# Kernel optimization log

Measured on AMD Instinct MI355X. Metric: run time of the kernel, lower is better.

## Reference

```python
import jax, jax.numpy as jnp
import numpy as np

FC = 8  # heads_count
EPS = 1e-12  # torch F.normalize eps


def setup_inputs() -> dict:
    key = jax.random.key(0)
    ks = jax.random.split(key, 8)
    n, l, s, C, H = 4, 4096, 256, 256, 256
    return {
        "x0": jax.random.normal(ks[0], (n, l, C), jnp.float32),
        "center1": jax.random.normal(ks[1], (n, s, C), jnp.float32),
        "W0": jax.random.normal(ks[2], (H, C), jnp.float32) * 0.05,
        "b0": jax.random.normal(ks[3], (H,), jnp.float32) * 0.05,
        "W1": jax.random.normal(ks[4], (2 * H, C), jnp.float32) * 0.05,
        "b1": jax.random.normal(ks[5], (2 * H,), jnp.float32) * 0.05,
        "Wm": jax.random.normal(ks[6], (C, H), jnp.float32) * 0.05,
        "bm": jax.random.normal(ks[7], (C,), jnp.float32) * 0.05,
        "alpha": jnp.ones((1,), jnp.float32),
        "beta": jnp.zeros((1,), jnp.float32),
    }


def _l2norm(x):
    # matches torch F.normalize(dim=-1): x / max(||x||, eps)
    nrm = jnp.sqrt(jnp.sum(x * x, axis=-1, keepdims=True))
    return x / jnp.maximum(nrm, EPS)


def reference(x0, center1, W0, b0, W1, b1, Wm, bm, alpha, beta):
    n, l, c = x0.shape
    s = center1.shape[1]
    H = W0.shape[0]
    sc = H // FC
    m = n * FC
    # projections
    x0p = x0 @ W0.T + b0                        # [n, l, H]
    c1 = center1 @ W1.T + b1                    # [n, s, 2H]
    # split heads: 'n l (fc sc) -> (n fc) l sc'
    x0p = x0p.reshape(n, l, FC, sc).transpose(0, 2, 1, 3).reshape(m, l, sc)
    c1 = c1.reshape(n, s, FC, 2 * sc).transpose(0, 2, 1, 3).reshape(m, s, 2 * sc)
    c_point, c_value = c1[..., :sc], c1[..., sc:]
    # cosine similarity + affine + sigmoid
    sim = jnp.einsum('mlc,msc->mls', _l2norm(x0p), _l2norm(c_point))
    sim = jax.nn.sigmoid(alpha[0] * sim + beta[0])
    # top-1 hard routing
    max_vals = jnp.max(sim, axis=2)             # [m, l]
    max_idx = jnp.argmax(sim, axis=2)           # [m, l]
    gathered = jnp.take_along_axis(c_value, max_idx[:, :, None], axis=1)  # [m, l, sc]
    dispatched = max_vals[:, :, None] * gathered
    # '(n fc) l sc -> n l (fc sc)'
    dispatched = dispatched.reshape(n, FC, l, sc).transpose(0, 2, 1, 3).reshape(n, l, H)
    return dispatched @ Wm.T + bm               # [n, l, c]
```

## Files before the change

### kernel.cpp

```cpp
#include <hip/hip_runtime.h>
#include <math.h>

#define Nn 4
#define Ll 4096
#define Ss 256
#define Cc 256
#define FC 8
#define SC 32

typedef __attribute__((ext_vector_type(8))) short short8;
typedef __attribute__((ext_vector_type(8))) _Float16 half8;
typedef __attribute__((ext_vector_type(4))) float f32x4;

__device__ __forceinline__ unsigned short f2bf(float x) {
  unsigned int u = __float_as_uint(x);
  return (unsigned short)((u + 0x7FFFu + ((u >> 16) & 1u)) >> 16);
}

__device__ __forceinline__ void split8v(float4 a, float4 b,
                                        half8& hi, half8& lo) {
  float v[8] = {a.x, a.y, a.z, a.w, b.x, b.y, b.z, b.w};
#pragma unroll
  for (int i = 0; i < 8; i++) {
    float x = v[i];
    _Float16 h = (_Float16)x;
    float r = (x - (float)h) * 2048.f;
    hi[i] = h;
    lo[i] = (_Float16)r;
  }
}

#define PROJ_LOAD(Abuf, Bbuf, KOFF)                                     \
  {                                                                     \
    _Pragma("unroll")                                                   \
    for (int mi = 0; mi < 4; mi++) {                                    \
      const float* p = Ab + (size_t)mi * 16 * Cc + (KOFF);              \
      Abuf[mi][0] = *(const float4*)p;                                  \
      Abuf[mi][1] = *(const float4*)(p + 4);                            \
    }                                                                   \
    _Pragma("unroll")                                                   \
    for (int ni = 0; ni < 2; ni++) {                                    \
      const float* p = Bb + (size_t)ni * 16 * Cc + (KOFF);              \
      Bbuf[ni][0] = *(const float4*)p;                                  \
      Bbuf[ni][1] = *(const float4*)(p + 4);                            \
    }                                                                   \
  }

#define PROJ_COMPUTE(Abuf, Bbuf)                                        \
  {                                                                     \
    half8 Bh[2], Bl[2];                                                 \
    _Pragma("unroll")                                                   \
    for (int ni = 0; ni < 2; ni++)                                      \
      split8v(Bbuf[ni][0], Bbuf[ni][1], Bh[ni], Bl[ni]);                \
    _Pragma("unroll")                                                   \
    for (int mi = 0; mi < 4; mi++) {                                    \
      half8 Ah, Al;                                                     \
      split8v(Abuf[mi][0], Abuf[mi][1], Ah, Al);                        \
      _Pragma("unroll")                                                 \
      for (int ni = 0; ni < 2; ni++) {                                  \
        acc1[mi][ni] = __builtin_amdgcn_mfma_f32_16x16x32_f16(          \
            Ah, Bh[ni], acc1[mi][ni], 0, 0, 0);                         \
        acc2[mi][ni] = __builtin_amdgcn_mfma_f32_16x16x32_f16(          \
            Ah, Bl[ni], acc2[mi][ni], 0, 0, 0);                         \
        acc2[mi][ni] = __builtin_amdgcn_mfma_f32_16x16x32_f16(          \
            Al, Bh[ni], acc2[mi][ni], 0, 0, 0);                         \
      }                                                                 \
    }                                                                   \
  }

__device__ __forceinline__ void mfma_core_f32(
    const float* __restrict__ A, const float* __restrict__ B,
    const float* __restrict__ bias, size_t m0w, int n0w, int lane,
    f32x4 acc1[4][2], f32x4 acc2[4][2]) {
  int quad = lane >> 4, l15 = lane & 15;
#pragma unroll
  for (int ni = 0; ni < 2; ni++) {
    float bv = bias[n0w + ni * 16 + l15];
    f32x4 ci = {bv, bv, bv, bv};
    f32x4 zz = {0.f, 0.f, 0.f, 0.f};
#pragma unroll
    for (int mi = 0; mi < 4; mi++) { acc1[mi][ni] = ci; acc2[mi][ni] = zz; }
  }
  const float* Ab = A + (m0w + l15) * Cc + quad * 8;
  const float* Bb = B + (size_t)(n0w + l15) * Cc + quad * 8;

  float4 cA[4][2], cB[2][2], nA[4][2], nB[2][2];
  PROJ_LOAD(cA, cB, 0);
#pragma unroll 1
  for (int kt = 0; kt < 8; kt += 2) {
    PROJ_LOAD(nA, nB, (kt + 1) * 32);
    PROJ_COMPUTE(cA, cB);
    if (kt < 6) PROJ_LOAD(cA, cB, (kt + 2) * 32);
    PROJ_COMPUTE(nA, nB);
  }
}

__global__ __launch_bounds__(256, 2) void proj_mfma_k(
    const float* __restrict__ x0, const float* __restrict__ W0,
    const float* __restrict__ b0, const float* __restrict__ center1,
    const float* __restrict__ W1, const float* __restrict__ b1,
    float* __restrict__ xn, float* __restrict__ cpn, float* __restrict__ cval) {
  int t = threadIdx.x;
  int wave = t >> 6, lane = t & 63;
  int quad = lane >> 4, l15 = lane & 15;
  int b = blockIdx.x;
  f32x4 acc1[4][2], acc2[4][2];

  if (b < 512) {
    int r = (b & 7) + 8 * ((b >> 3) & 15);
    int cb = b >> 7;
    size_t m0 = (size_t)r * 128 + (size_t)(wave & 1) * 64;
    int n0 = cb * 64 + (wave >> 1) * 32;
    mfma_core_f32(x0, W0, b0, m0, n0, lane, acc1, acc2);
#pragma unroll
    for (int mi = 0; mi < 4; mi++) {
#pragma unroll
      for (int reg = 0; reg < 4; reg++) {
        size_t row = m0 + mi * 16 + quad * 4 + reg;
        float* orow = xn + row * Cc + n0;
#pragma unroll
        for (int ni = 0; ni < 2; ni++)
          orow[ni * 16 + l15] =
              acc1[mi][ni][reg] + acc2[mi][ni][reg] * (1.f / 2048.f);
      }
    }
  } else {
    int b2 = b - 512;
    size_t m0 = (size_t)(b2 >> 3) * 128 + (size_t)(wave & 1) * 64;
    int n0 = (b2 & 7) * 64 + (wave >> 1) * 32;
    mfma_core_f32(center1, W1, b1, m0, n0, lane, acc1, acc2);
    int f = n0 >> 6;
    bool point = (n0 & 32) == 0;
#pragma unroll
    for (int mi = 0; mi < 4; mi++) {
#pragma unroll
      for (int reg = 0; reg < 4; reg++) {
        int row = (int)m0 + mi * 16 + quad * 4 + reg;
        int nI = row >> 8, s = row & 255;
        float v0 = acc1[mi][0][reg] + acc2[mi][0][reg] * (1.f / 2048.f);
        float v1 = acc1[mi][1][reg] + acc2[mi][1][reg] * (1.f / 2048.f);
        size_t base = (((size_t)nI * FC + f) * Ss + s) * SC;
        if (point) {
          float ss = v0 * v0 + v1 * v1;
          ss += __shfl_xor(ss, 1, 64);
          ss += __shfl_xor(ss, 2, 64);
          ss += __shfl_xor(ss, 4, 64);
          ss += __shfl_xor(ss, 8, 64);
          float rin = 1.f / fmaxf(sqrtf(ss), 1e-12f);
          cpn[base + l15] = v0 * rin;
          cpn[base + 16 + l15] = v1 * rin;
        } else {
          cval[base + l15] = v0;
          cval[base + 16 + l15] = v1;
        }
      }
    }
  }
}

__global__ __launch_bounds__(256) void sim_k(
    float* __restrict__ xn, const float* __restrict__ cpn,
    const float* __restrict__ cval, const float* __restrict__ alphap,
    const float* __restrict__ betap) {
  __shared__ half8 BhS[4][256];
  __shared__ half8 BlS[4][256];
  int t = threadIdx.x;
  int wave = t >> 6, lane = t & 63;
  int quad = lane >> 4, l15 = lane & 15;
  int lt = blockIdx.x & 63;
  int nf = blockIdx.x >> 6;
  int f = nf & 7, nI = nf >> 3;
  int l0 = lt * 64;
  const float* cp = cpn + (size_t)nf * Ss * SC;

  {
    int s = t;
    float4 va[8];
#pragma unroll
    for (int q8 = 0; q8 < 8; q8++)
      va[q8] = *(const float4*)(cp + (size_t)s * SC + q8 * 4);
#pragma unroll
    for (int q = 0; q < 4; q++) {
      half8 h, l;
      split8v(va[2 * q], va[2 * q + 1], h, l);
      BhS[q][s] = h;
      BlS[q][s] = l;
    }
  }

  half8 Ah, Al;
  {
    const float* xrow =
        xn + ((size_t)nI * Ll + l0 + wave * 16 + l15) * Cc + f * SC + quad * 8;
    float4 a0 = *(const float4*)xrow;
    float4 a1 = *(const float4*)(xrow + 4);
    float ssq = a0.x * a0.x + a0.y * a0.y + a0.z * a0.z + a0.w * a0.w +
                a1.x * a1.x + a1.y * a1.y + a1.z * a1.z + a1.w * a1.w;
    ssq += __shfl_xor(ssq, 16, 64);
    ssq += __shfl_xor(ssq, 32, 64);
    float rin = 1.f / fmaxf(sqrtf(ssq), 1e-12f);
    a0.x *= rin; a0.y *= rin; a0.z *= rin; a0.w *= rin;
    a1.x *= rin; a1.y *= rin; a1.z *= rin; a1.w *= rin;
    split8v(a0, a1, Ah, Al);
  }

  __syncthreads();

  float a = alphap[0], bt = betap[0];
  float best[4];
  int bi[4];
#pragma unroll
  for (int r = 0; r < 4; r++) { best[r] = -3.0e38f; bi[r] = 0; }

#pragma unroll
  for (int j = 0; j < 16; j++) {
    half8 bh = BhS[quad][j * 16 + l15];
    half8 bl = BlS[quad][j * 16 + l15];
    f32x4 z = {0.f, 0.f, 0.f, 0.f};
    f32x4 c1 = __builtin_amdgcn_mfma_f32_16x16x32_f16(Ah, bh, z, 0, 0, 0);
    f32x4 c2 = __builtin_amdgcn_mfma_f32_16x16x32_f16(Ah, bl, z, 0, 0, 0);
    c2 = __builtin_amdgcn_mfma_f32_16x16x32_f16(Al, bh, c2, 0, 0, 0);
    int s = j * 16 + l15;
#pragma unroll
    for (int r = 0; r < 4; r++) {
      float v = c1[r] + c2[r] * (1.f / 2048.f);
      float tv = fmaf(a, v, bt);
      if (tv > best[r]) { best[r] = tv; bi[r] = s; }
    }
  }

#pragma unroll
  for (int r = 0; r < 4; r++) {
    float bv = best[r];
    int ix = bi[r];
#pragma unroll
    for (int m = 1; m <= 8; m <<= 1) {
      float ov = __shfl_xor(bv, m, 64);
      int oi = __shfl_xor(ix, m, 64);
      if (ov > bv || (ov == bv && oi < ix)) { bv = ov; ix = oi; }
    }
    float mv = 1.f / (1.f + expf(-bv));
    const float* cvp = cval + ((size_t)nf * Ss + ix) * SC;
    float* orow =
        xn + ((size_t)nI * Ll + l0 + wave * 16 + quad * 4 + r) * Cc + f * SC;
    orow[l15] = cvp[l15] * mv;
    orow[l15 + 16] = cvp[l15 + 16] * mv;
  }
}

__global__ __launch_bounds__(256) void out_mfma_k(
    const float* __restrict__ xn, const float* __restrict__ Wm,
    const float* __restrict__ bm, float* __restrict__ out) {
  int t = threadIdx.x;
  int wave = t >> 6, lane = t & 63;
  int quad = lane >> 4, l15 = lane & 15;
  size_t m0 = (size_t)(blockIdx.x >> 1) * 128 + (wave & 1) * 64;
  int n0 = (blockIdx.x & 1) * 128 + (wave >> 1) * 64;

  f32x4 acc[4][4];
#pragma unroll
  for (int ni = 0; ni < 4; ni++) {
    float bv = bm[n0 + ni * 16 + l15];
    f32x4 ci = {bv, bv, bv, bv};
#pragma unroll
    for (int mi = 0; mi < 4; mi++) acc[mi][ni] = ci;
  }

  for (int kt = 0; kt < 8; kt++) {
    int k0 = kt * 32 + quad * 8;
    short8 Af[4], Bf[4];
#pragma unroll
    for (int mi = 0; mi < 4; mi++) {
      const float* p = xn + (m0 + mi * 16 + l15) * Cc + k0;
      float4 lo = *(const float4*)p;
      float4 hi = *(const float4*)(p + 4);
      short8 fr;
      fr[0] = (short)f2bf(lo.x); fr[1] = (short)f2bf(lo.y);
      fr[2] = (short)f2bf(lo.z); fr[3] = (short)f2bf(lo.w);
      fr[4] = (short)f2bf(hi.x); fr[5] = (short)f2bf(hi.y);
      fr[6] = (short)f2bf(hi.z); fr[7] = (short)f2bf(hi.w);
      Af[mi] = fr;
    }
#pragma unroll
    for (int ni = 0; ni < 4; ni++) {
      const float* p = Wm + (size_t)(n0 + ni * 16 + l15) * Cc + k0;
      float4 lo = *(const float4*)p;
      float4 hi = *(const float4*)(p + 4);
      short8 fr;
      fr[0] = (short)f2bf(lo.x); fr[1] = (short)f2bf(lo.y);
      fr[2] = (short)f2bf(lo.z); fr[3] = (short)f2bf(lo.w);
      fr[4] = (short)f2bf(hi.x); fr[5] = (short)f2bf(hi.y);
      fr[6] = (short)f2bf(hi.z); fr[7] = (short)f2bf(hi.w);
      Bf[ni] = fr;
    }
#pragma unroll
    for (int mi = 0; mi < 4; mi++)
#pragma unroll
      for (int ni = 0; ni < 4; ni++)
        acc[mi][ni] = __builtin_amdgcn_mfma_f32_16x16x32_bf16(
            Af[mi], Bf[ni], acc[mi][ni], 0, 0, 0);
  }

#pragma unroll
  for (int mi = 0; mi < 4; mi++) {
#pragma unroll
    for (int reg = 0; reg < 4; reg++) {
      size_t row = m0 + mi * 16 + quad * 4 + reg;
      float* orow = out + row * Cc + n0;
#pragma unroll
      for (int ni = 0; ni < 4; ni++)
        orow[ni * 16 + l15] = acc[mi][ni][reg];
    }
  }
}

extern "C" void kernel_launch(void* const* d_in, const int* in_sizes, int n_in,
                              void* d_out, int out_size, void* d_ws, size_t ws_size,
                              hipStream_t stream) {
  const float* x0      = (const float*)d_in[0];
  const float* center1 = (const float*)d_in[1];
  const float* W0      = (const float*)d_in[2];
  const float* b0      = (const float*)d_in[3];
  const float* W1      = (const float*)d_in[4];
  const float* b1      = (const float*)d_in[5];
  const float* Wm      = (const float*)d_in[6];
  const float* bm      = (const float*)d_in[7];
  const float* alpha   = (const float*)d_in[8];
  const float* beta    = (const float*)d_in[9];
  float* out = (float*)d_out;
  float* ws  = (float*)d_ws;

  float* xn   = ws;
  float* cpn  = xn + (size_t)Nn * Ll * Cc;
  float* cval = cpn + (size_t)Nn * FC * Ss * SC;

  proj_mfma_k<<<dim3(576), dim3(256), 0, stream>>>(
      x0, W0, b0, center1, W1, b1, xn, cpn, cval);
  sim_k<<<dim3(32 * 64), dim3(256), 0, stream>>>(xn, cpn, cval, alpha, beta);
  out_mfma_k<<<dim3(256), dim3(256), 0, stream>>>(xn, Wm, bm, out);
}
```

Baseline: 161.8 us.

## Stage projection GEMM operands through swizzled LDS with async global_load_lds

```diff
diff --git a/kernel.cpp b/kernel.cpp
--- a/kernel.cpp
+++ b/kernel.cpp
@@ -30,49 +30,95 @@
   }
 }
 
-#define PROJ_LOAD(Abuf, Bbuf, KOFF)                                     \
-  {                                                                     \
-    _Pragma("unroll")                                                   \
-    for (int mi = 0; mi < 4; mi++) {                                    \
-      const float* p = Ab + (size_t)mi * 16 * Cc + (KOFF);              \
-      Abuf[mi][0] = *(const float4*)p;                                  \
-      Abuf[mi][1] = *(const float4*)(p + 4);                            \
-    }                                                                   \
-    _Pragma("unroll")                                                   \
-    for (int ni = 0; ni < 2; ni++) {                                    \
-      const float* p = Bb + (size_t)ni * 16 * Cc + (KOFF);              \
-      Bbuf[ni][0] = *(const float4*)p;                                  \
-      Bbuf[ni][1] = *(const float4*)(p + 4);                            \
-    }                                                                   \
-  }
-
-#define PROJ_COMPUTE(Abuf, Bbuf)                                        \
-  {                                                                     \
-    half8 Bh[2], Bl[2];                                                 \
-    _Pragma("unroll")                                                   \
-    for (int ni = 0; ni < 2; ni++)                                      \
-      split8v(Bbuf[ni][0], Bbuf[ni][1], Bh[ni], Bl[ni]);                \
-    _Pragma("unroll")                                                   \
-    for (int mi = 0; mi < 4; mi++) {                                    \
-      half8 Ah, Al;                                                     \
-      split8v(Abuf[mi][0], Abuf[mi][1], Ah, Al);                        \
-      _Pragma("unroll")                                                 \
-      for (int ni = 0; ni < 2; ni++) {                                  \
-        acc1[mi][ni] = __builtin_amdgcn_mfma_f32_16x16x32_f16(          \
-            Ah, Bh[ni], acc1[mi][ni], 0, 0, 0);                         \
-        acc2[mi][ni] = __builtin_amdgcn_mfma_f32_16x16x32_f16(          \
-            Ah, Bl[ni], acc2[mi][ni], 0, 0, 0);                         \
-        acc2[mi][ni] = __builtin_amdgcn_mfma_f32_16x16x32_f16(          \
-            Al, Bh[ni], acc2[mi][ni], 0, 0, 0);                         \
-      }                                                                 \
-    }                                                                   \
-  }
-
-__device__ __forceinline__ void mfma_core_f32(
-    const float* __restrict__ A, const float* __restrict__ B,
-    const float* __restrict__ bias, size_t m0w, int n0w, int lane,
-    f32x4 acc1[4][2], f32x4 acc2[4][2]) {
+#define STAGE(Abuf, Bbuf, K0)                                               \
+  {                                                                         \
+    _Pragma("unroll")                                                       \
+    for (int j = 0; j < 4; j++) {                                           \
+      int c = wave * 4 + j;                                                 \
+      const float* g = Ag + (m0blk + 8 * c + lr) * Cc + (K0) + scol;        \
+      __builtin_amdgcn_global_load_lds(                                     \
+          (const __attribute__((address_space(1))) void*)g,                 \
+          (__attribute__((address_space(3))) void*)((Abuf) + c * 256),      \
+          16, 0, 0);                                                        \
+    }                                                                       \
+    _Pragma("unroll")                                                       \
+    for (int j = 0; j < 2; j++) {                                           \
+      int c = wave * 2 + j;                                                 \
+      const float* g =                                                      \
+          Bg + (size_t)(n0blk + 8 * c + lr) * Cc + (K0) + scol;             \
+      __builtin_amdgcn_global_load_lds(                                     \
+          (const __attribute__((address_space(1))) void*)g,                 \
+          (__attribute__((address_space(3))) void*)((Bbuf) + c * 256),      \
+          16, 0, 0);                                                        \
+    }                                                                       \
+  }
+
+#define KSTEP(Ac, Bc)                                                       \
+  {                                                                         \
+    half8 Bh[2], Bl[2];                                                     \
+    _Pragma("unroll")                                                       \
+    for (int ni = 0; ni < 2; ni++) {                                        \
+      int rw = bR0 + ni * 16 + l15;                                         \
+      int rb = rw * 32, xs = rw & 7;                                        \
+      float4 f0 = *(const float4*)&(Bc)[rb + (((quad * 2) ^ xs) << 2)];     \
+      float4 f1 = *(const float4*)&(Bc)[rb + (((quad * 2 + 1) ^ xs) << 2)]; \
+      split8v(f0, f1, Bh[ni], Bl[ni]);                                      \
+    }                                                                       \
+    _Pragma("unroll")                                                       \
+    for (int mi = 0; mi < 4; mi++) {                                        \
+      int rw = aR0 + mi * 16 + l15;                                         \
+      int rb = rw * 32, xs = rw & 7;                                        \
+      float4 f0 = *(const float4*)&(Ac)[rb + (((quad * 2) ^ xs) << 2)];     \
+      float4 f1 = *(const float4*)&(Ac)[rb + (((quad * 2 + 1) ^ xs) << 2)]; \
+      half8 Ah, Al;                                                         \
+      split8v(f0, f1, Ah, Al);                                              \
+      _Pragma("unroll")                                                     \
+      for (int ni = 0; ni < 2; ni++) {                                      \
+        acc1[mi][ni] = __builtin_amdgcn_mfma_f32_16x16x32_f16(              \
+            Ah, Bh[ni], acc1[mi][ni], 0, 0, 0);                             \
+        acc2[mi][ni] = __builtin_amdgcn_mfma_f32_16x16x32_f16(              \
+            Ah, Bl[ni], acc2[mi][ni], 0, 0, 0);                             \
+        acc2[mi][ni] = __builtin_amdgcn_mfma_f32_16x16x32_f16(              \
+            Al, Bh[ni], acc2[mi][ni], 0, 0, 0);                             \
+      }                                                                     \
+    }                                                                       \
+  }
+
+__global__ __launch_bounds__(256) void proj_mfma_k(
+    const float* __restrict__ x0, const float* __restrict__ W0,
+    const float* __restrict__ b0, const float* __restrict__ center1,
+    const float* __restrict__ W1, const float* __restrict__ b1,
+    float* __restrict__ xn, float* __restrict__ cpn, float* __restrict__ cval) {
+  __shared__ float As[2][128 * 32];
+  __shared__ float Bs[2][64 * 32];
+  int t = threadIdx.x;
+  int wave = t >> 6, lane = t & 63;
   int quad = lane >> 4, l15 = lane & 15;
+  int l8 = lane & 7, lr = lane >> 3;
+  int scol = (l8 ^ lr) << 2;
+  int b = blockIdx.x;
+
+  const float *Ag, *Bg, *bias;
+  size_t m0blk;
+  int n0blk;
+  bool isX = (b < 512);
+  if (isX) {
+    int rt = b & 127, cb = b >> 7;
+    m0blk = (size_t)rt * 128;
+    n0blk = cb * 64;
+    Ag = x0; Bg = W0; bias = b0;
+  } else {
+    int b2 = b - 512;
+    m0blk = (size_t)(b2 >> 3) * 128;
+    n0blk = (b2 & 7) * 64;
+    Ag = center1; Bg = W1; bias = b1;
+  }
+
+  int n0w = n0blk + (wave >> 1) * 32;
+  int aR0 = (wave & 1) * 64;
+  int bR0 = (wave >> 1) * 32;
+
+  f32x4 acc1[4][2], acc2[4][2];
 #pragma unroll
   for (int ni = 0; ni < 2; ni++) {
     float bv = bias[n0w + ni * 16 + l15];
@@ -81,43 +127,35 @@
 #pragma unroll
     for (int mi = 0; mi < 4; mi++) { acc1[mi][ni] = ci; acc2[mi][ni] = zz; }
   }
-  const float* Ab = A + (m0w + l15) * Cc + quad * 8;
-  const float* Bb = B + (size_t)(n0w + l15) * Cc + quad * 8;
-
-  float4 cA[4][2], cB[2][2], nA[4][2], nB[2][2];
-  PROJ_LOAD(cA, cB, 0);
+
+  float* Ac = &As[0][0]; float* An = &As[1][0];
+  float* Bc = &Bs[0][0]; float* Bn = &Bs[1][0];
+  STAGE(Ac, Bc, 0);
 #pragma unroll 1
-  for (int kt = 0; kt < 8; kt += 2) {
-    PROJ_LOAD(nA, nB, (kt + 1) * 32);
-    PROJ_COMPUTE(cA, cB);
-    if (kt < 6) PROJ_LOAD(cA, cB, (kt + 2) * 32);
-    PROJ_COMPUTE(nA, nB);
-  }
-}
-
-__global__ __launch_bounds__(256, 2) void proj_mfma_k(
-    const float* __restrict__ x0, const float* __restrict__ W0,
-    const float* __restrict__ b0, const float* __restrict__ center1,
-    const float* __restrict__ W1, const float* __restrict__ b1,
-    float* __restrict__ xn, float* __restrict__ cpn, float* __restrict__ cval) {
-  int t = threadIdx.x;
-  int wave = t >> 6, lane = t & 63;
-  int quad = lane >> 4, l15 = lane & 15;
-  int b = blockIdx.x;
-  f32x4 acc1[4][2], acc2[4][2];
-
-  if (b < 512) {
-    int r = (b & 7) + 8 * ((b >> 3) & 15);
-    int cb = b >> 7;
-    size_t m0 = (size_t)r * 128 + (size_t)(wave & 1) * 64;
-    int n0 = cb * 64 + (wave >> 1) * 32;
-    mfma_core_f32(x0, W0, b0, m0, n0, lane, acc1, acc2);
+  for (int kt = 0; kt < 8; kt++) {
+    if (kt < 7) {
+      STAGE(An, Bn, (kt + 1) * 32);
+      asm volatile("s_waitcnt vmcnt(6)" ::: "memory");
+    } else {
+      asm volatile("s_waitcnt vmcnt(0)" ::: "memory");
+    }
+    __builtin_amdgcn_sched_barrier(0);
+    __syncthreads();
+    KSTEP(Ac, Bc);
+    __syncthreads();
+    float* tp;
+    tp = Ac; Ac = An; An = tp;
+    tp = Bc; Bc = Bn; Bn = tp;
+  }
+
+  if (isX) {
+    size_t m0 = m0blk + aR0;
 #pragma unroll
     for (int mi = 0; mi < 4; mi++) {
 #pragma unroll
       for (int reg = 0; reg < 4; reg++) {
         size_t row = m0 + mi * 16 + quad * 4 + reg;
-        float* orow = xn + row * Cc + n0;
+        float* orow = xn + row * Cc + n0w;
 #pragma unroll
         for (int ni = 0; ni < 2; ni++)
           orow[ni * 16 + l15] =
@@ -125,17 +163,14 @@
       }
     }
   } else {
-    int b2 = b - 512;
-    size_t m0 = (size_t)(b2 >> 3) * 128 + (size_t)(wave & 1) * 64;
-    int n0 = (b2 & 7) * 64 + (wave >> 1) * 32;
-    mfma_core_f32(center1, W1, b1, m0, n0, lane, acc1, acc2);
-    int f = n0 >> 6;
-    bool point = (n0 & 32) == 0;
+    int f = n0w >> 6;
+    bool point = (n0w & 32) == 0;
+    int m0 = (int)m0blk + aR0;
 #pragma unroll
     for (int mi = 0; mi < 4; mi++) {
 #pragma unroll
       for (int reg = 0; reg < 4; reg++) {
-        int row = (int)m0 + mi * 16 + quad * 4 + reg;
+        int row = m0 + mi * 16 + quad * 4 + reg;
         int nI = row >> 8, s = row & 255;
         float v0 = acc1[mi][0][reg] + acc2[mi][0][reg] * (1.f / 2048.f);
         float v1 = acc1[mi][1][reg] + acc2[mi][1][reg] * (1.f / 2048.f);
```

Measured after the change: 149.5 us. 7.6% less time.
